# Performance work log

Measured on AMD Instinct MI355X. Metric: run time of the kernel, lower is better.

## Reference

```python
import jax, jax.numpy as jnp
import numpy as np

K_KNOW = 50000   # know_length
E_KNOW = 128     # know_emb_size
T_TOPIC = 512    # topic_size
H_SEQ = 512      # seq_hidden_size
D_IN = T_TOPIC + 1  # GRU input size in 'concat' score_mode


def setup_inputs() -> dict:
    key = jax.random.key(0)
    ks = jax.random.split(key, 11)
    return {
        "o_e": jax.random.normal(ks[0], (E_KNOW,), dtype=jnp.float32),
        "ex_e": jax.random.normal(ks[1], (T_TOPIC,), dtype=jnp.float32),
        "s": jax.random.uniform(ks[2], (1,), dtype=jnp.float32),
        "h": jax.random.normal(ks[3], (1, K_KNOW, H_SEQ), dtype=jnp.float32) * 0.1,
        "knowledge_memory": jax.random.uniform(ks[4], (K_KNOW, E_KNOW), dtype=jnp.float32, minval=-1.0, maxval=1.0),
        "W_ih": jax.random.normal(ks[5], (3 * H_SEQ, D_IN), dtype=jnp.float32) * 0.04,
        "W_hh": jax.random.normal(ks[6], (3 * H_SEQ, H_SEQ), dtype=jnp.float32) * 0.04,
        "b_ih": jax.random.normal(ks[7], (3 * H_SEQ,), dtype=jnp.float32) * 0.04,
        "b_hh": jax.random.normal(ks[8], (3 * H_SEQ,), dtype=jnp.float32) * 0.04,
        "score_W": jax.random.normal(ks[9], (1, T_TOPIC + H_SEQ), dtype=jnp.float32) * 0.03,
        "score_b": jax.random.normal(ks[10], (1,), dtype=jnp.float32),
    }


def reference(o_e, ex_e, s, h, knowledge_memory, W_ih, W_hh, b_ih, b_hh, score_W, score_b):
    K, H = knowledge_memory.shape[0], h.shape[-1]
    h2 = h.reshape(K, H)                      # [K, H]
    # attention over external knowledge memory
    alpha = knowledge_memory @ o_e            # [K]
    beta = jax.nn.softmax(alpha)              # [K]
    # weighted read of hidden state
    hkp = beta @ h2                           # [H]
    # score head
    pred_v = jnp.concatenate([ex_e, hkp])     # [T+H]
    predict_score = score_W @ pred_v + score_b  # [1]
    # GRU input ('concat' mode): x = [ex_e, s], broadcast-weighted by beta
    x = jnp.concatenate([ex_e, s])            # [D_IN]
    xk = beta[:, None] * x[None, :]           # [K, D_IN]
    # single-step GRU cell (torch GRU semantics)
    gi = xk @ W_ih.T + b_ih                   # [K, 3H]
    gh = h2 @ W_hh.T + b_hh                   # [K, 3H]
    i_r, i_z, i_n = jnp.split(gi, 3, axis=1)
    h_r, h_z, h_n = jnp.split(gh, 3, axis=1)
    r = jax.nn.sigmoid(i_r + h_r)
    z = jax.nn.sigmoid(i_z + h_z)
    n = jnp.tanh(i_n + r * h_n)
    h_new = (1.0 - z) * n + z * h2            # [K, H]
    return predict_score.reshape(1), h_new[None]  # ([1], [1, K, H])
```

## Files before the change

kernel.cpp:

```cpp
#include <hip/hip_runtime.h>

#define KK 50000
#define EE 128
#define HH 512
#define DIN 513

typedef short bh8 __attribute__((ext_vector_type(8)));
typedef float fx16 __attribute__((ext_vector_type(16)));

__device__ __forceinline__ short f2b(float f) {
  unsigned u = __float_as_uint(f);
  u = u + 0x7fffu + ((u >> 16) & 1u);
  return (short)(u >> 16);
}
__device__ __forceinline__ float b2f(short b) {
  return __uint_as_float(((unsigned)(unsigned short)b) << 16);
}
__device__ __forceinline__ float sigm(float x) { return 1.f / (1.f + __expf(-x)); }
__device__ __forceinline__ float tanh_(float x) {
  float ax = fabsf(x);
  float e = __expf(-2.f * ax);
  float t = (1.f - e) / (1.f + e);
  return copysignf(t, x);
}

__global__ void k_alpha(const float* __restrict__ km, const float* __restrict__ oe,
                        float* __restrict__ alpha) {
  int t = blockIdx.x * 256 + threadIdx.x;
  int r = t >> 4, j = t & 15;
  if (r >= KK) return;
  const float4* p = (const float4*)(km + (size_t)r * EE + j * 8);
  const float4* q = (const float4*)(oe + j * 8);
  float4 a0 = p[0], a1 = p[1], b0 = q[0], b1 = q[1];
  float s = a0.x * b0.x + a0.y * b0.y + a0.z * b0.z + a0.w * b0.w
          + a1.x * b1.x + a1.y * b1.y + a1.z * b1.z + a1.w * b1.w;
  s += __shfl_xor(s, 1); s += __shfl_xor(s, 2);
  s += __shfl_xor(s, 4); s += __shfl_xor(s, 8);
  if (j == 0) alpha[r] = s;
}

__global__ void k_wpack(const float* __restrict__ whh, short* __restrict__ bp) {
  int o = blockIdx.x * 256 + threadIdx.x;
  int n = o & 511;
  int gk = o >> 9;
  int g = gk >> 6, cb = gk & 63;
  const float* src = whh + ((size_t)(g * 512 + n)) * 512 + cb * 8;
  float4 f0 = *(const float4*)src;
  float4 f1 = *(const float4*)(src + 4);
  bh8 w;
  w[0] = f2b(f0.x); w[1] = f2b(f0.y); w[2] = f2b(f0.z); w[3] = f2b(f0.w);
  w[4] = f2b(f1.x); w[5] = f2b(f1.y); w[6] = f2b(f1.z); w[7] = f2b(f1.w);
  *(bh8*)(bp + (size_t)o * 8) = w;
}

__global__ void k_gix(const float* __restrict__ wih, const float* __restrict__ exe,
                      const float* __restrict__ sv, float* __restrict__ gix,
                      float* __restrict__ hkp) {
  int t = threadIdx.x;
  if (blockIdx.x < 2) {
    int g = blockIdx.x * 256 + t;
    hkp[g] = 0.f;
  }
  int w = blockIdx.x * 4 + (t >> 6);
  int lane = t & 63;
  float s1 = sv[0];
  float sum = 0.f;
  for (int d = lane; d < DIN; d += 64) {
    float xv = (d < 512) ? exe[d] : s1;
    sum += wih[(size_t)w * DIN + d] * xv;
  }
  sum += __shfl_xor(sum, 1); sum += __shfl_xor(sum, 2);
  sum += __shfl_xor(sum, 4); sum += __shfl_xor(sum, 8);
  sum += __shfl_xor(sum, 16); sum += __shfl_xor(sum, 32);
  if (lane == 0) gix[w] = sum;
}

__global__ void k_softmax(const float* __restrict__ alpha, float* __restrict__ beta) {
  __shared__ float red[16];
  __shared__ float stat[2];
  int t = threadIdx.x;
  float m = -1e30f;
  for (int i = t; i < KK; i += 1024) m = fmaxf(m, alpha[i]);
  for (int o = 1; o < 64; o <<= 1) m = fmaxf(m, __shfl_xor(m, o));
  if ((t & 63) == 0) red[t >> 6] = m;
  __syncthreads();
  if (t == 0) {
    float mm = red[0];
    for (int i = 1; i < 16; ++i) mm = fmaxf(mm, red[i]);
    stat[0] = mm;
  }
  __syncthreads();
  float Mx = stat[0];
  float ss = 0.f;
  for (int i = t; i < KK; i += 1024) ss += __expf(alpha[i] - Mx);
  for (int o = 1; o < 64; o <<= 1) ss += __shfl_xor(ss, o);
  if ((t & 63) == 0) red[t >> 6] = ss;
  __syncthreads();
  if (t == 0) {
    float tot = 0.f;
    for (int i = 0; i < 16; ++i) tot += red[i];
    stat[1] = tot;
  }
  __syncthreads();
  float inv = 1.f / stat[1];
  for (int i = t; i < KK; i += 1024) beta[i] = __expf(alpha[i] - Mx) * inv;
}

__global__ __launch_bounds__(512, 2) void k_gemm(
    const float* __restrict__ h, const float* __restrict__ beta,
    const float* __restrict__ gix, const float* __restrict__ b_ih,
    const float* __restrict__ b_hh, const short* __restrict__ bp,
    float* __restrict__ hkp, float* __restrict__ out) {
  __shared__ short Abuf[64 * 1040];
  __shared__ float hk[512];
  const int t = threadIdx.x;
  const int r0 = blockIdx.x * 128;
  hk[t] = 0.f;

  const int kb = t & 63;
  const int wid = t >> 6;
  float hp[8] = {0.f, 0.f, 0.f, 0.f, 0.f, 0.f, 0.f, 0.f};
  #pragma unroll 2
  for (int pass = 0; pass < 16; ++pass) {
    const int r = pass * 8 + wid;
    const int gr = r0 + r;
    float v[8];
    float bv = 0.f;
    if (gr < KK) {
      const float4* p = (const float4*)(h + (size_t)gr * HH + kb * 8);
      float4 x0 = p[0], x1 = p[1];
      v[0] = x0.x; v[1] = x0.y; v[2] = x0.z; v[3] = x0.w;
      v[4] = x1.x; v[5] = x1.y; v[6] = x1.z; v[7] = x1.w;
      bv = beta[gr];
    } else {
      #pragma unroll
      for (int j = 0; j < 8; ++j) v[j] = 0.f;
    }
    bh8 w;
    #pragma unroll
    for (int j = 0; j < 8; ++j) { hp[j] += bv * v[j]; w[j] = f2b(v[j]); }
    *(bh8*)&Abuf[kb * 1040 + r * 8] = w;
  }
  __syncthreads();
  #pragma unroll
  for (int j = 0; j < 8; ++j) atomicAdd(&hk[kb * 8 + j], hp[j]);
  __syncthreads();
  atomicAdd(&hkp[t], hk[t]);

  const int lane = t & 63;
  const int l31 = lane & 31;
  const int lh = lane >> 5;
  const int wm = wid >> 2;
  const int wn = wid & 3;
  const int abase = lh * 1040 + (wm * 64 + l31) * 8;
  float* out1 = out + 1;

  for (int ni = 0; ni < 4; ++ni) {
    const int col = ni * 128 + wn * 32 + l31;
    const short* bpc = bp + ((size_t)(lh * 512 + col)) * 8;
    fx16 acc[2][3];
    #pragma unroll
    for (int mi = 0; mi < 2; ++mi)
      #pragma unroll
      for (int g = 0; g < 3; ++g)
        #pragma unroll
        for (int q = 0; q < 16; ++q) acc[mi][g][q] = 0.f;

    bh8 bA[3], bB[3];
    auto LDB = [&](bh8* d, int s) {
      d[0] = *(const bh8*)(bpc + (size_t)s * 8192);
      d[1] = *(const bh8*)(bpc + 262144 + (size_t)s * 8192);
      d[2] = *(const bh8*)(bpc + 524288 + (size_t)s * 8192);
    };
    LDB(bA, 0);
    #pragma unroll 4
    for (int s2 = 0; s2 < 16; ++s2) {
      const int s0 = 2 * s2, s1 = 2 * s2 + 1;
      LDB(bB, s1);
      bh8 a0 = *(const bh8*)&Abuf[abase + s0 * 2080];
      bh8 a1 = *(const bh8*)&Abuf[abase + s0 * 2080 + 256];
      acc[0][0] = __builtin_amdgcn_mfma_f32_32x32x16_bf16(a0, bA[0], acc[0][0], 0, 0, 0);
      acc[0][1] = __builtin_amdgcn_mfma_f32_32x32x16_bf16(a0, bA[1], acc[0][1], 0, 0, 0);
      acc[0][2] = __builtin_amdgcn_mfma_f32_32x32x16_bf16(a0, bA[2], acc[0][2], 0, 0, 0);
      acc[1][0] = __builtin_amdgcn_mfma_f32_32x32x16_bf16(a1, bA[0], acc[1][0], 0, 0, 0);
      acc[1][1] = __builtin_amdgcn_mfma_f32_32x32x16_bf16(a1, bA[1], acc[1][1], 0, 0, 0);
      acc[1][2] = __builtin_amdgcn_mfma_f32_32x32x16_bf16(a1, bA[2], acc[1][2], 0, 0, 0);
      if (s2 < 15) LDB(bA, s0 + 2);
      a0 = *(const bh8*)&Abuf[abase + s1 * 2080];
      a1 = *(const bh8*)&Abuf[abase + s1 * 2080 + 256];
      acc[0][0] = __builtin_amdgcn_mfma_f32_32x32x16_bf16(a0, bB[0], acc[0][0], 0, 0, 0);
      acc[0][1] = __builtin_amdgcn_mfma_f32_32x32x16_bf16(a0, bB[1], acc[0][1], 0, 0, 0);
      acc[0][2] = __builtin_amdgcn_mfma_f32_32x32x16_bf16(a0, bB[2], acc[0][2], 0, 0, 0);
      acc[1][0] = __builtin_amdgcn_mfma_f32_32x32x16_bf16(a1, bB[0], acc[1][0], 0, 0, 0);
      acc[1][1] = __builtin_amdgcn_mfma_f32_32x32x16_bf16(a1, bB[1], acc[1][1], 0, 0, 0);
      acc[1][2] = __builtin_amdgcn_mfma_f32_32x32x16_bf16(a1, bB[2], acc[1][2], 0, 0, 0);
    }

    const int cb = col >> 3, c7 = col & 7;
    const float gxr = gix[col], gxz = gix[col + 512], gxn = gix[col + 1024];
    const float bir = b_ih[col], biz = b_ih[col + 512], bin = b_ih[col + 1024];
    const float bhr = b_hh[col], bhz = b_hh[col + 512], bhn = b_hh[col + 1024];
    #pragma unroll
    for (int mi = 0; mi < 2; ++mi) {
      const int lrb = wm * 64 + mi * 32 + 4 * lh;
      #pragma unroll
      for (int q = 0; q < 16; ++q) {
        const int lr = lrb + (q & 3) + 8 * (q >> 2);
        const int gr = r0 + lr;
        if (gr < KK) {
          const float bv = beta[gr];
          const float rv = sigm(acc[mi][0][q] + bv * gxr + bir + bhr);
          const float zv = sigm(acc[mi][1][q] + bv * gxz + biz + bhz);
          const float nv = tanh_(bv * gxn + bin + rv * (acc[mi][2][q] + bhn));
          const float ho = b2f(Abuf[cb * 1040 + lr * 8 + c7]);
          out1[(size_t)gr * HH + col] = (1.f - zv) * nv + zv * ho;
        }
      }
    }
  }
}

__global__ void k_score(const float* __restrict__ sw, const float* __restrict__ sb,
                        const float* __restrict__ exe, const float* __restrict__ hkp,
                        float* __restrict__ out) {
  __shared__ float red[8];
  int t = threadIdx.x;
  float v = sw[t] * exe[t] + sw[512 + t] * hkp[t];
  for (int o = 1; o < 64; o <<= 1) v += __shfl_xor(v, o);
  if ((t & 63) == 0) red[t >> 6] = v;
  __syncthreads();
  if (t == 0) {
    float s = sb[0];
    for (int i = 0; i < 8; ++i) s += red[i];
    out[0] = s;
  }
}

extern "C" void kernel_launch(void* const* d_in, const int* in_sizes, int n_in,
                              void* d_out, int out_size, void* d_ws, size_t ws_size,
                              hipStream_t stream) {
  const float* o_e  = (const float*)d_in[0];
  const float* ex_e = (const float*)d_in[1];
  const float* s    = (const float*)d_in[2];
  const float* h    = (const float*)d_in[3];
  const float* km   = (const float*)d_in[4];
  const float* W_ih = (const float*)d_in[5];
  const float* W_hh = (const float*)d_in[6];
  const float* b_ih = (const float*)d_in[7];
  const float* b_hh = (const float*)d_in[8];
  const float* sW   = (const float*)d_in[9];
  const float* sb   = (const float*)d_in[10];
  float* out = (float*)d_out;

  float* wsf   = (float*)d_ws;
  float* alpha = wsf;
  float* beta  = wsf + 50048;
  float* gix   = wsf + 100096;
  float* hkp   = wsf + 101632;
  short* bp    = (short*)(wsf + 102400);

  k_alpha<<<3125, 256, 0, stream>>>(km, o_e, alpha);
  k_wpack<<<384, 256, 0, stream>>>(W_hh, bp);
  k_gix<<<384, 256, 0, stream>>>(W_ih, ex_e, s, gix, hkp);
  k_softmax<<<1, 1024, 0, stream>>>(alpha, beta);
  k_gemm<<<391, 512, 0, stream>>>(h, beta, gix, b_ih, b_hh, bp, hkp, out);
  k_score<<<1, 512, 0, stream>>>(sW, sb, ex_e, hkp, out);
}
```

Baseline: 234.2 us.

## Halve GEMM row tile to 64 and deepen B-operand prefetch for occupancy

The fused GRU GEMM kernel now handles 64 rows per block instead of 128. That halves LDS usage and the per-wave accumulators, lets launch bounds ask for 4 blocks per CU, and doubles the grid. The B-fragment loads from the packed W_hh now use a 4-deep rotating prefetch. Beta is cached in LDS for the epilogue instead of being re-read from global memory. In exchange, each block reuses every B fragment for half as many rows, so W_hh reads from L2 double, and the hkp atomics double with the block count.

Result: slower. 406.3 us (+73.5%).

```diff
diff --git a/kernel.cpp b/kernel.cpp
--- a/kernel.cpp
+++ b/kernel.cpp
@@ -106,22 +106,23 @@
   for (int i = t; i < KK; i += 1024) beta[i] = __expf(alpha[i] - Mx) * inv;
 }
 
-__global__ __launch_bounds__(512, 2) void k_gemm(
+__global__ __launch_bounds__(512, 4) void k_gemm(
     const float* __restrict__ h, const float* __restrict__ beta,
     const float* __restrict__ gix, const float* __restrict__ b_ih,
     const float* __restrict__ b_hh, const short* __restrict__ bp,
     float* __restrict__ hkp, float* __restrict__ out) {
-  __shared__ short Abuf[64 * 1040];
+  __shared__ short Abuf[64 * 520];
   __shared__ float hk[512];
+  __shared__ float Lbeta[64];
   const int t = threadIdx.x;
-  const int r0 = blockIdx.x * 128;
+  const int r0 = blockIdx.x * 64;
   hk[t] = 0.f;
 
   const int kb = t & 63;
   const int wid = t >> 6;
   float hp[8] = {0.f, 0.f, 0.f, 0.f, 0.f, 0.f, 0.f, 0.f};
   #pragma unroll 2
-  for (int pass = 0; pass < 16; ++pass) {
+  for (int pass = 0; pass < 8; ++pass) {
     const int r = pass * 8 + wid;
     const int gr = r0 + r;
     float v[8];
@@ -136,10 +137,11 @@
       #pragma unroll
       for (int j = 0; j < 8; ++j) v[j] = 0.f;
     }
+    if (kb == 0) Lbeta[r] = bv;
     bh8 w;
     #pragma unroll
     for (int j = 0; j < 8; ++j) { hp[j] += bv * v[j]; w[j] = f2b(v[j]); }
-    *(bh8*)&Abuf[kb * 1040 + r * 8] = w;
+    *(bh8*)&Abuf[kb * 520 + r * 8] = w;
   }
   __syncthreads();
   #pragma unroll
@@ -152,69 +154,55 @@
   const int lh = lane >> 5;
   const int wm = wid >> 2;
   const int wn = wid & 3;
-  const int abase = lh * 1040 + (wm * 64 + l31) * 8;
+  const short* Ab = &Abuf[lh * 520 + (wm * 32 + l31) * 8];
   float* out1 = out + 1;
 
   for (int ni = 0; ni < 4; ++ni) {
     const int col = ni * 128 + wn * 32 + l31;
     const short* bpc = bp + ((size_t)(lh * 512 + col)) * 8;
-    fx16 acc[2][3];
+    fx16 acc0, acc1, acc2;
     #pragma unroll
-    for (int mi = 0; mi < 2; ++mi)
-      #pragma unroll
-      for (int g = 0; g < 3; ++g)
-        #pragma unroll
-        for (int q = 0; q < 16; ++q) acc[mi][g][q] = 0.f;
-
-    bh8 bA[3], bB[3];
-    auto LDB = [&](bh8* d, int s) {
-      d[0] = *(const bh8*)(bpc + (size_t)s * 8192);
-      d[1] = *(const bh8*)(bpc + 262144 + (size_t)s * 8192);
-      d[2] = *(const bh8*)(bpc + 524288 + (size_t)s * 8192);
+    for (int q = 0; q < 16; ++q) { acc0[q] = 0.f; acc1[q] = 0.f; acc2[q] = 0.f; }
+
+    bh8 b0[3], b1[3], b2[3], b3[3];
+    auto LDB3 = [&](bh8* d, int sp) {
+      d[0] = *(const bh8*)(bpc + (size_t)sp * 8192);
+      d[1] = *(const bh8*)(bpc + 262144 + (size_t)sp * 8192);
+      d[2] = *(const bh8*)(bpc + 524288 + (size_t)sp * 8192);
     };
-    LDB(bA, 0);
-    #pragma unroll 4
-    for (int s2 = 0; s2 < 16; ++s2) {
-      const int s0 = 2 * s2, s1 = 2 * s2 + 1;
-      LDB(bB, s1);
-      bh8 a0 = *(const bh8*)&Abuf[abase + s0 * 2080];
-      bh8 a1 = *(const bh8*)&Abuf[abase + s0 * 2080 + 256];
-      acc[0][0] = __builtin_amdgcn_mfma_f32_32x32x16_bf16(a0, bA[0], acc[0][0], 0, 0, 0);
-      acc[0][1] = __builtin_amdgcn_mfma_f32_32x32x16_bf16(a0, bA[1], acc[0][1], 0, 0, 0);
-      acc[0][2] = __builtin_amdgcn_mfma_f32_32x32x16_bf16(a0, bA[2], acc[0][2], 0, 0, 0);
-      acc[1][0] = __builtin_amdgcn_mfma_f32_32x32x16_bf16(a1, bA[0], acc[1][0], 0, 0, 0);
-      acc[1][1] = __builtin_amdgcn_mfma_f32_32x32x16_bf16(a1, bA[1], acc[1][1], 0, 0, 0);
-      acc[1][2] = __builtin_amdgcn_mfma_f32_32x32x16_bf16(a1, bA[2], acc[1][2], 0, 0, 0);
-      if (s2 < 15) LDB(bA, s0 + 2);
-      a0 = *(const bh8*)&Abuf[abase + s1 * 2080];
-      a1 = *(const bh8*)&Abuf[abase + s1 * 2080 + 256];
-      acc[0][0] = __builtin_amdgcn_mfma_f32_32x32x16_bf16(a0, bB[0], acc[0][0], 0, 0, 0);
-      acc[0][1] = __builtin_amdgcn_mfma_f32_32x32x16_bf16(a0, bB[1], acc[0][1], 0, 0, 0);
-      acc[0][2] = __builtin_amdgcn_mfma_f32_32x32x16_bf16(a0, bB[2], acc[0][2], 0, 0, 0);
-      acc[1][0] = __builtin_amdgcn_mfma_f32_32x32x16_bf16(a1, bB[0], acc[1][0], 0, 0, 0);
-      acc[1][1] = __builtin_amdgcn_mfma_f32_32x32x16_bf16(a1, bB[1], acc[1][1], 0, 0, 0);
-      acc[1][2] = __builtin_amdgcn_mfma_f32_32x32x16_bf16(a1, bB[2], acc[1][2], 0, 0, 0);
+    auto STEP = [&](int s, const bh8* cur, bh8* nxt) {
+      bh8 a = *(const bh8*)(Ab + s * 1040);
+      acc0 = __builtin_amdgcn_mfma_f32_32x32x16_bf16(a, cur[0], acc0, 0, 0, 0);
+      acc1 = __builtin_amdgcn_mfma_f32_32x32x16_bf16(a, cur[1], acc1, 0, 0, 0);
+      acc2 = __builtin_amdgcn_mfma_f32_32x32x16_bf16(a, cur[2], acc2, 0, 0, 0);
+      LDB3(nxt, (s + 3) & 31);
+    };
+    LDB3(b0, 0);
+    LDB3(b1, 1);
+    LDB3(b2, 2);
+    for (int u = 0; u < 32; u += 4) {
+      STEP(u + 0, b0, b3);
+      STEP(u + 1, b1, b0);
+      STEP(u + 2, b2, b1);
+      STEP(u + 3, b3, b2);
     }
 
     const int cb = col >> 3, c7 = col & 7;
     const float gxr = gix[col], gxz = gix[col + 512], gxn = gix[col + 1024];
     const float bir = b_ih[col], biz = b_ih[col + 512], bin = b_ih[col + 1024];
     const float bhr = b_hh[col], bhz = b_hh[col + 512], bhn = b_hh[col + 1024];
+    const int lrb = wm * 32 + 4 * lh;
     #pragma unroll
-    for (int mi = 0; mi < 2; ++mi) {
-      const int lrb = wm * 64 + mi * 32 + 4 * lh;
-      #pragma unroll
-      for (int q = 0; q < 16; ++q) {
-        const int lr = lrb + (q & 3) + 8 * (q >> 2);
-        const int gr = r0 + lr;
-        if (gr < KK) {
-          const float bv = beta[gr];
-          const float rv = sigm(acc[mi][0][q] + bv * gxr + bir + bhr);
-          const float zv = sigm(acc[mi][1][q] + bv * gxz + biz + bhz);
-          const float nv = tanh_(bv * gxn + bin + rv * (acc[mi][2][q] + bhn));
-          const float ho = b2f(Abuf[cb * 1040 + lr * 8 + c7]);
-          out1[(size_t)gr * HH + col] = (1.f - zv) * nv + zv * ho;
-        }
+    for (int q = 0; q < 16; ++q) {
+      const int lr = lrb + (q & 3) + 8 * (q >> 2);
+      const int gr = r0 + lr;
+      if (gr < KK) {
+        const float bv = Lbeta[lr];
+        const float rv = sigm(acc0[q] + bv * gxr + bir + bhr);
+        const float zv = sigm(acc1[q] + bv * gxz + biz + bhz);
+        const float nv = tanh_(bv * gxn + bin + rv * (acc2[q] + bhn));
+        const float ho = b2f(Abuf[cb * 520 + lr * 8 + c7]);
+        out1[(size_t)gr * HH + col] = (1.f - zv) * nv + zv * ho;
       }
     }
   }
@@ -263,6 +251,6 @@
   k_wpack<<<384, 256, 0, stream>>>(W_hh, bp);
   k_gix<<<384, 256, 0, stream>>>(W_ih, ex_e, s, gix, hkp);
   k_softmax<<<1, 1024, 0, stream>>>(alpha, beta);
-  k_gemm<<<391, 512, 0, stream>>>(h, beta, gix, b_ih, b_hh, bp, hkp, out);
+  k_gemm<<<782, 512, 0, stream>>>(h, beta, gix, b_ih, b_hh, bp, hkp, out);
   k_score<<<1, 512, 0, stream>>>(sW, sb, ex_e, hkp, out);
 }
```
